# Performance work log

Measured on AMD Instinct MI355X. Metric: run time of the kernel, lower is better.

The kernel has to match this reference:

```python
import jax, jax.numpy as jnp
import numpy as np

V, E, H, L = 50000, 300, 256, 5
B, T_C, T_T = 64, 637, 24


def _lstm_dir(x, wih, whh, b, reverse):
    # x: [B,T,E]; wih: [4H,E]; whh: [4H,H]; b: [4H]
    pre = jnp.einsum('bte,ge->btg', x, wih) + b  # [B,T,4H]
    h0 = jnp.zeros((x.shape[0], whh.shape[1]), x.dtype)

    def step(carry, p):
        h, c = carry
        g = p + h @ whh.T
        i, f, gg, o = jnp.split(g, 4, axis=-1)
        c = jax.nn.sigmoid(f) * c + jax.nn.sigmoid(i) * jnp.tanh(gg)
        h = jax.nn.sigmoid(o) * jnp.tanh(c)
        return (h, c), h

    _, hs = jax.lax.scan(step, (h0, h0), jnp.swapaxes(pre, 0, 1), reverse=reverse)
    return jnp.swapaxes(hs, 0, 1)  # [B,T,H]


def _bilstm(x, wih_f, whh_f, b_f, wih_b, whh_b, b_b):
    return jnp.concatenate([
        _lstm_dir(x, wih_f, whh_f, b_f, False),
        _lstm_dir(x, wih_b, whh_b, b_b, True),
    ], axis=-1)  # [B,T,2H]


def setup_inputs() -> dict:
    key = jax.random.key(0)
    ks = jax.random.split(key, 20)
    k = 1.0 / np.sqrt(H)
    u = lambda kk, shape: jax.random.uniform(kk, shape, jnp.float32, -k, k)
    inp = {
        'content': jax.random.randint(ks[0], (B, T_C), 0, V),
        'title': jax.random.randint(ks[1], (B, T_T), 0, V),
        'embed_w': jax.random.normal(ks[2], (V, E), jnp.float32),
        't_wih_f': u(ks[3], (4 * H, E)), 't_whh_f': u(ks[4], (4 * H, H)), 't_b_f': u(ks[5], (4 * H,)),
        't_wih_b': u(ks[6], (4 * H, E)), 't_whh_b': u(ks[7], (4 * H, H)), 't_b_b': u(ks[8], (4 * H,)),
        'c_wih_f': u(ks[9], (4 * H, E)), 'c_whh_f': u(ks[10], (4 * H, H)), 'c_b_f': u(ks[11], (4 * H,)),
        'c_wih_b': u(ks[12], (4 * H, E)), 'c_whh_b': u(ks[13], (4 * H, H)), 'c_b_b': u(ks[14], (4 * H,)),
        'att_w': u(ks[15], (2 * H, 2 * H)),
        'fc_w': u(ks[16], (L, T_C)), 'fc_b': u(ks[17], (L,)),
    }
    return inp


def reference(content, title, embed_w, t_wih_f, t_whh_f, t_b_f, t_wih_b, t_whh_b, t_b_b,
              c_wih_f, c_whh_f, c_b_f, c_wih_b, c_whh_b, c_b_b, att_w, fc_w, fc_b):
    content_embed = embed_w[content]  # [B,Tc,E]
    title_embed = embed_w[title]      # [B,Tt,E]
    title_rep = _bilstm(title_embed, t_wih_f, t_whh_f, t_b_f, t_wih_b, t_whh_b, t_b_b)
    content_rep = _bilstm(content_embed, c_wih_f, c_whh_f, c_b_f, c_wih_b, c_whh_b, c_b_b)
    title_last = title_rep[:, -1, :]  # [B,2H]
    # score[b,t] = title_last[b] . (att_w @ content_rep[b,t])  (Linear with weight att_w: x @ att_w.T)
    a = jnp.einsum('bj,jk,btk->bt', title_last, att_w, content_rep)  # [B,Tc]
    a = jax.nn.softmax(a, axis=1)
    return jax.nn.log_softmax(a @ fc_w.T + fc_b, axis=1)  # [B,L]
```

## Files before the change

kernel.cpp:

```cpp
#include <hip/hip_runtime.h>
#include <stdint.h>

typedef __attribute__((ext_vector_type(8))) short bf16x8v;
typedef __attribute__((ext_vector_type(4))) float f32x4v;
typedef long long i64;

#define DEV static __device__ __forceinline__

#define B_   64
#define TC_  637
#define TCP_ 638
#define TT_  24
#define E_   300
#define KP_  320
#define H_   256
#define NG_  2048

DEV uint16_t f2bf(float f) {
    uint32_t u = __float_as_uint(f);
    u += 0x7fffu + ((u >> 16) & 1u);
    return (uint16_t)(u >> 16);
}
DEV float bf2f(uint16_t h) { return __uint_as_float(((uint32_t)h) << 16); }
DEV float sigm(float x)  { return __builtin_amdgcn_rcpf(1.f + __builtin_amdgcn_exp2f(x * -1.4426950408889634f)); }
DEV float tanhx(float x) { return 1.f - 2.f*__builtin_amdgcn_rcpf(1.f + __builtin_amdgcn_exp2f(x * 2.8853900817779268f)); }

DEV void gload_lds16(const void* g, void* l) {
    __builtin_amdgcn_global_load_lds((const __attribute__((address_space(1))) uint32_t*)g,
                                     (__attribute__((address_space(3))) uint32_t*)l, 16, 0, 0);
}

__global__ void k_prep(const float* t_wih_f, const float* t_wih_b,
                       const float* t_whh_f,
                       const float* c_wih_f, const float* c_wih_b,
                       const float* c_whh_f, const float* c_whh_b,
                       const float* t_b_f, const float* t_b_b,
                       const float* c_b_f, const float* c_b_b,
                       uint16_t* BwC, uint16_t* BwT, float* biasC, float* biasT,
                       uint32_t* w8CF, uint32_t* w8CB, uint32_t* w8TF)
{
    int tid = blockIdx.x*blockDim.x + threadIdx.x;
    int nth = gridDim.x*blockDim.x;
    for (int i = tid; i < NG_*KP_; i += nth) {
        int n = i / KP_, k = i - n*KP_;
        float vc = 0.f, vt = 0.f;
        if (k < E_) {
            vc = (n < 1024) ? c_wih_f[n*E_+k] : c_wih_b[(n-1024)*E_+k];
            vt = (n < 1024) ? t_wih_f[n*E_+k] : t_wih_b[(n-1024)*E_+k];
        }
        BwC[i] = f2bf(vc); BwT[i] = f2bf(vt);
    }
    for (int i = tid; i < 1024*H_/4; i += nth) {
        int base = i*4;
        uint32_t a, b, c;
        a = (uint32_t)__builtin_amdgcn_cvt_pk_fp8_f32(c_whh_f[base], c_whh_f[base+1], 0, false);
        a = (uint32_t)__builtin_amdgcn_cvt_pk_fp8_f32(c_whh_f[base+2], c_whh_f[base+3], (int)a, true);
        b = (uint32_t)__builtin_amdgcn_cvt_pk_fp8_f32(c_whh_b[base], c_whh_b[base+1], 0, false);
        b = (uint32_t)__builtin_amdgcn_cvt_pk_fp8_f32(c_whh_b[base+2], c_whh_b[base+3], (int)b, true);
        c = (uint32_t)__builtin_amdgcn_cvt_pk_fp8_f32(t_whh_f[base], t_whh_f[base+1], 0, false);
        c = (uint32_t)__builtin_amdgcn_cvt_pk_fp8_f32(t_whh_f[base+2], t_whh_f[base+3], (int)c, true);
        w8CF[i] = a; w8CB[i] = b; w8TF[i] = c;
    }
    for (int i = tid; i < NG_; i += nth) {
        biasC[i] = (i < 1024) ? c_b_f[i] : c_b_b[i-1024];
        biasT[i] = (i < 1024) ? t_b_f[i] : t_b_b[i-1024];
    }
}

__global__ void k_gather(const int* __restrict__ content, const int* __restrict__ title,
                         const float* __restrict__ emb,
                         uint16_t* __restrict__ Ac, uint16_t* __restrict__ At)
{
    int tid = blockIdx.x*blockDim.x + threadIdx.x;
    int nth = gridDim.x*blockDim.x;
    const int CCH = 40832*40;
    const int TCH = 1536*40;
    for (int i = tid; i < CCH + TCH; i += nth) {
        uint16_t* dst; int row, c8; int tok;
        if (i < CCH) {
            row = i / 40; c8 = i - row*40;
            int t = row >> 6, b = row & 63;
            tok = (t < TC_) ? content[b*TC_ + t] : -1;
            dst = Ac + (size_t)row*KP_ + c8*8;
        } else {
            int jx = i - CCH;
            row = jx / 40; c8 = jx - row*40;
            int t = row >> 6, b = row & 63;
            tok = title[b*TT_ + t];
            dst = At + (size_t)row*KP_ + c8*8;
        }
        uint32_t dd[4];
        #pragma unroll
        for (int p = 0; p < 4; ++p) {
            int k = c8*8 + p*2;
            float f0 = (tok >= 0 && k   < E_) ? emb[(size_t)tok*E_ + k]   : 0.f;
            float f1 = (tok >= 0 && k+1 < E_) ? emb[(size_t)tok*E_ + k+1] : 0.f;
            dd[p] = (uint32_t)f2bf(f0) | ((uint32_t)f2bf(f1) << 16);
        }
        uint4 q; q.x = dd[0]; q.y = dd[1]; q.z = dd[2]; q.w = dd[3];
        *(uint4*)dst = q;
    }
}

__global__ __launch_bounds__(256) void k_gemm(const uint16_t* __restrict__ A,
        const uint16_t* __restrict__ Bw, const float* __restrict__ bias,
        uint16_t* __restrict__ prep)
{
    __shared__ __align__(16) uint16_t lA[2][128*32];
    __shared__ __align__(16) uint16_t lB[2][128*32];
    const int tid = threadIdx.x;
    const int l = tid & 63, wv = tid >> 6;
    const int m0 = blockIdx.y * 128, n0 = blockIdx.x * 128;

    auto stage = [&](int kc, int bi) {
        #pragma unroll
        for (int r = 0; r < 2; ++r) {
            int row = r*64 + (tid >> 2);
            int cu  = (tid & 3) * 8;
            gload_lds16(A  + (size_t)(m0 + row)*KP_ + kc*32 + cu, &lA[bi][r*2048 + wv*512]);
            gload_lds16(Bw + (size_t)(n0 + row)*KP_ + kc*32 + cu, &lB[bi][r*2048 + wv*512]);
        }
    };

    f32x4v acc[4][4];
    #pragma unroll
    for (int i = 0; i < 4; ++i)
        #pragma unroll
        for (int j = 0; j < 4; ++j)
            acc[i][j] = f32x4v{0.f,0.f,0.f,0.f};

    const int mtb = (wv >> 1) * 4, ntb = (wv & 1) * 4;

    stage(0, 0);
    __syncthreads();
    for (int kc = 0; kc < 10; ++kc) {
        if (kc < 9) stage(kc + 1, (kc + 1) & 1);
        {
            int bi = kc & 1;
            bf16x8v af[4], bfr[4];
            #pragma unroll
            for (int i = 0; i < 4; ++i) {
                af[i]  = *(const bf16x8v*)&lA[bi][((mtb+i)*16 + (l&15))*32 + (l>>4)*8];
                bfr[i] = *(const bf16x8v*)&lB[bi][((ntb+i)*16 + (l&15))*32 + (l>>4)*8];
            }
            #pragma unroll
            for (int i = 0; i < 4; ++i)
                #pragma unroll
                for (int j = 0; j < 4; ++j)
                    acc[i][j] = __builtin_amdgcn_mfma_f32_16x16x32_bf16(bfr[j], af[i], acc[i][j], 0,0,0);
        }
        __syncthreads();
    }

    const int hi = l >> 4;
    #pragma unroll
    for (int j = 0; j < 4; ++j) {
        int n16 = (n0 >> 4) + ntb + j;
        int dir = n16 >> 6;
        int q   = n16 & 63;
        int ty  = q >> 4;
        int wp  = q & 15;
        float4 bv = *(const float4*)(bias + n16*16 + hi*4);
        #pragma unroll
        for (int i = 0; i < 4; ++i) {
            int rowblk = (m0 >> 4) + mtb + i;
            int t    = rowblk >> 2;
            int bblk = rowblk & 3;
            int unit = t*8 + bblk*2 + dir;
            ushort4 pk;
            pk.x = f2bf(acc[i][j][0] + bv.x);
            pk.y = f2bf(acc[i][j][1] + bv.y);
            pk.z = f2bf(acc[i][j][2] + bv.z);
            pk.w = f2bf(acc[i][j][3] + bv.w);
            size_t off = (size_t)unit*16384 + (size_t)wp*1024 + (size_t)l*16 + ty*4;
            *(ushort4*)(prep + off) = pk;
        }
    }
}

__global__ __launch_bounds__(1024, 4) void k_rnn(
    const uint16_t* __restrict__ preC, const uint16_t* __restrict__ preT,
    const uint8_t* __restrict__ w8CF, const uint8_t* __restrict__ w8CB,
    const uint8_t* __restrict__ w8TF,
    uint16_t* __restrict__ cr, float* __restrict__ tl)
{
    __shared__ __align__(16) char smem[8192];

    const int tid = threadIdx.x;
    const int l = tid & 63, wp = tid >> 6;
    const int m = l & 15, hi = l >> 4;
    const int u = blockIdx.x;

    int dir, bblk, t0, tstep, nsteps, tlOff = -1;
    bool doCR = false;
    const uint16_t* pre; const uint8_t* whh8 = nullptr;
    if (u < 8) {
        dir = u & 1; bblk = u >> 1;
        nsteps = TC_; t0 = dir ? (TC_-1) : 0; tstep = dir ? -1 : 1;
        whh8 = dir ? w8CB : w8CF; pre = preC; doCR = true;
    } else if (u < 12) {
        dir = 0; bblk = u - 8; nsteps = TT_; t0 = 0; tstep = 1;
        whh8 = w8TF; pre = preT; tlOff = 0;
    } else {
        dir = 1; bblk = u - 12; nsteps = 1; t0 = TT_-1; tstep = -1;
        whh8 = nullptr; pre = preT; tlOff = 256;
    }
    const int b0 = bblk * 16;

    i64 w8r[4][8];
    if (whh8) {
        #pragma unroll
        for (int ty = 0; ty < 4; ++ty) {
            int n = ty*256 + wp*16 + m;
            #pragma unroll
            for (int kc = 0; kc < 8; ++kc)
                w8r[ty][kc] = *(const i64*)(whh8 + (size_t)n*H_ + kc*32 + hi*8);
        }
        #pragma unroll
        for (int ty = 0; ty < 4; ++ty)
            #pragma unroll
            for (int kc = 0; kc < 8; ++kc)
                asm volatile("" : "+a"(w8r[ty][kc]));
    }
    for (int i = tid; i < 2048; i += 1024) ((uint32_t*)smem)[i] = 0;
    __syncthreads();

    const int sw = (m & 3) << 5;
    const int rdBase = m*256 + hi*8;
    const int wa = m*256 + (((wp << 4) + hi*4) ^ sw);
    uint16_t* crp = cr + ((size_t)(b0 + m)*TC_ + t0)*512 + dir*256 + (wp << 4) + hi*4;
    const intptr_t crAdv = (intptr_t)tstep * 512;

    float cst[4] = {0.f, 0.f, 0.f, 0.f};

    const uint16_t* pp = pre + (size_t)(t0*8 + bblk*2 + dir)*16384
                             + (size_t)(wp << 10) + (size_t)l*16;
    const intptr_t ppAdv = (intptr_t)tstep * 131072;

    uint4 pf0 = *(const uint4*)(pp);
    uint4 pf1 = *(const uint4*)(pp + 8);

    for (int s = 0; s < nsteps; ++s) {
        const char* hb = (const char*)smem + (s & 1)*4096;
        char*       ho = smem + ((s & 1) ^ 1)*4096;

        f32x4v acc[4];
        acc[0][0]=__uint_as_float(pf0.x<<16); acc[0][1]=__uint_as_float(pf0.x&0xffff0000u);
        acc[0][2]=__uint_as_float(pf0.y<<16); acc[0][3]=__uint_as_float(pf0.y&0xffff0000u);
        acc[1][0]=__uint_as_float(pf0.z<<16); acc[1][1]=__uint_as_float(pf0.z&0xffff0000u);
        acc[1][2]=__uint_as_float(pf0.w<<16); acc[1][3]=__uint_as_float(pf0.w&0xffff0000u);
        acc[2][0]=__uint_as_float(pf1.x<<16); acc[2][1]=__uint_as_float(pf1.x&0xffff0000u);
        acc[2][2]=__uint_as_float(pf1.y<<16); acc[2][3]=__uint_as_float(pf1.y&0xffff0000u);
        acc[3][0]=__uint_as_float(pf1.z<<16); acc[3][1]=__uint_as_float(pf1.z&0xffff0000u);
        acc[3][2]=__uint_as_float(pf1.w<<16); acc[3][3]=__uint_as_float(pf1.w&0xffff0000u);

        if (s + 1 < nsteps) {
            pp += ppAdv;
            pf0 = *(const uint4*)(pp);
            pf1 = *(const uint4*)(pp + 8);
        }

        if (whh8) {
            #pragma unroll
            for (int kc = 0; kc < 8; ++kc) {
                i64 a8 = *(const i64*)(hb + rdBase + ((kc << 5) ^ sw));
                asm("v_mfma_f32_16x16x32_fp8_fp8 %0, %1, %2, %0"
                    : "+v"(acc[0]) : "a"(w8r[0][kc]), "v"(a8));
                asm("v_mfma_f32_16x16x32_fp8_fp8 %0, %1, %2, %0"
                    : "+v"(acc[1]) : "a"(w8r[1][kc]), "v"(a8));
                asm("v_mfma_f32_16x16x32_fp8_fp8 %0, %1, %2, %0"
                    : "+v"(acc[2]) : "a"(w8r[2][kc]), "v"(a8));
                asm("v_mfma_f32_16x16x32_fp8_fp8 %0, %1, %2, %0"
                    : "+v"(acc[3]) : "a"(w8r[3][kc]), "v"(a8));
            }
        }

        float hv0, hv1, hv2, hv3;
        {
            float si, sf, tg, so, cv;
            si = sigm(acc[0][0]); sf = sigm(acc[1][0]); tg = tanhx(acc[2][0]); so = sigm(acc[3][0]);
            cv = sf*cst[0] + si*tg; cst[0] = cv; hv0 = so*tanhx(cv);
            si = sigm(acc[0][1]); sf = sigm(acc[1][1]); tg = tanhx(acc[2][1]); so = sigm(acc[3][1]);
            cv = sf*cst[1] + si*tg; cst[1] = cv; hv1 = so*tanhx(cv);
            si = sigm(acc[0][2]); sf = sigm(acc[1][2]); tg = tanhx(acc[2][2]); so = sigm(acc[3][2]);
            cv = sf*cst[2] + si*tg; cst[2] = cv; hv2 = so*tanhx(cv);
            si = sigm(acc[0][3]); sf = sigm(acc[1][3]); tg = tanhx(acc[2][3]); so = sigm(acc[3][3]);
            cv = sf*cst[3] + si*tg; cst[3] = cv; hv3 = so*tanhx(cv);
        }
        uint32_t p8 = (uint32_t)__builtin_amdgcn_cvt_pk_fp8_f32(hv0, hv1, 0, false);
        p8 = (uint32_t)__builtin_amdgcn_cvt_pk_fp8_f32(hv2, hv3, (int)p8, true);
        *(uint32_t*)(ho + wa) = p8;

        if (doCR) {
            uint32_t b01, b23;
            asm("v_cvt_pk_bf16_f32 %0, %1, %2" : "=v"(b01) : "v"(hv0), "v"(hv1));
            asm("v_cvt_pk_bf16_f32 %0, %1, %2" : "=v"(b23) : "v"(hv2), "v"(hv3));
            uint2 st; st.x = b01; st.y = b23;
            *(uint2*)crp = st;
            crp += crAdv;
        }
        if (tlOff >= 0 && s == nsteps - 1) {
            float4 fv; fv.x = hv0; fv.y = hv1; fv.z = hv2; fv.w = hv3;
            *(float4*)(tl + (size_t)(b0 + m)*512 + tlOff + (wp << 4) + hi*4) = fv;
        }

        __builtin_amdgcn_sched_barrier(0);
        asm volatile("s_waitcnt lgkmcnt(0)" ::: "memory");
        __builtin_amdgcn_s_barrier();
        __builtin_amdgcn_sched_barrier(0);
    }
}

__global__ __launch_bounds__(256) void k_attn(const uint16_t* __restrict__ cr,
        const float* __restrict__ tl, const float* __restrict__ attw,
        const float* __restrict__ fcw, const float* __restrict__ fcb,
        float* __restrict__ out)
{
    __shared__ float sT[512];
    __shared__ float sQ[512];
    __shared__ float sS[640];
    __shared__ float sR[256];
    const int b = blockIdx.x, tid = threadIdx.x;
    for (int i = tid; i < 512; i += 256) sT[i] = tl[(size_t)b*512 + i];
    __syncthreads();
    for (int n = tid; n < 512; n += 256) {
        float s = 0.f;
        for (int j = 0; j < 512; ++j) s += sT[j] * attw[(size_t)j*512 + n];
        sQ[n] = s;
    }
    __syncthreads();
    for (int t = tid; t < TC_; t += 256) {
        const uint16_t* row = cr + ((size_t)b*TC_ + t)*512;
        float s = 0.f;
        for (int c = 0; c < 64; ++c) {
            uint4 v = *(const uint4*)(row + c*8);
            uint32_t d;
            d = v.x; s += bf2f((uint16_t)(d&0xffff))*sQ[c*8+0] + bf2f((uint16_t)(d>>16))*sQ[c*8+1];
            d = v.y; s += bf2f((uint16_t)(d&0xffff))*sQ[c*8+2] + bf2f((uint16_t)(d>>16))*sQ[c*8+3];
            d = v.z; s += bf2f((uint16_t)(d&0xffff))*sQ[c*8+4] + bf2f((uint16_t)(d>>16))*sQ[c*8+5];
            d = v.w; s += bf2f((uint16_t)(d&0xffff))*sQ[c*8+6] + bf2f((uint16_t)(d>>16))*sQ[c*8+7];
        }
        sS[t] = s;
    }
    __syncthreads();
    float lm = -1e30f;
    for (int t = tid; t < TC_; t += 256) lm = fmaxf(lm, sS[t]);
    sR[tid] = lm; __syncthreads();
    for (int o = 128; o > 0; o >>= 1) { if (tid < o) sR[tid] = fmaxf(sR[tid], sR[tid+o]); __syncthreads(); }
    float M = sR[0]; __syncthreads();
    float ls = 0.f;
    for (int t = tid; t < TC_; t += 256) { float e = __expf(sS[t]-M); sS[t] = e; ls += e; }
    sR[tid] = ls; __syncthreads();
    for (int o = 128; o > 0; o >>= 1) { if (tid < o) sR[tid] += sR[tid+o]; __syncthreads(); }
    float inv = 1.f / sR[0]; __syncthreads();
    float la[5] = {0.f,0.f,0.f,0.f,0.f};
    for (int t = tid; t < TC_; t += 256) {
        float p = sS[t] * inv;
        #pragma unroll
        for (int ll = 0; ll < 5; ++ll) la[ll] += p * fcw[ll*TC_ + t];
    }
    float lg[5];
    #pragma unroll
    for (int ll = 0; ll < 5; ++ll) {
        sR[tid] = la[ll]; __syncthreads();
        for (int o = 128; o > 0; o >>= 1) { if (tid < o) sR[tid] += sR[tid+o]; __syncthreads(); }
        lg[ll] = sR[0] + fcb[ll]; __syncthreads();
    }
    if (tid == 0) {
        float m2 = lg[0];
        #pragma unroll
        for (int ll = 1; ll < 5; ++ll) m2 = fmaxf(m2, lg[ll]);
        float se = 0.f;
        #pragma unroll
        for (int ll = 0; ll < 5; ++ll) se += __expf(lg[ll] - m2);
        float lse = __logf(se) + m2;
        #pragma unroll
        for (int ll = 0; ll < 5; ++ll) out[b*5 + ll] = lg[ll] - lse;
    }
}

extern "C" void kernel_launch(void* const* d_in, const int* in_sizes, int n_in,
                              void* d_out, int out_size, void* d_ws, size_t ws_size,
                              hipStream_t stream)
{
    const int*   content = (const int*)d_in[0];
    const int*   title   = (const int*)d_in[1];
    const float* embed_w = (const float*)d_in[2];
    const float* t_wih_f = (const float*)d_in[3];
    const float* t_whh_f = (const float*)d_in[4];
    const float* t_b_f   = (const float*)d_in[5];
    const float* t_wih_b = (const float*)d_in[6];
    const float* t_b_b   = (const float*)d_in[8];
    const float* c_wih_f = (const float*)d_in[9];
    const float* c_whh_f = (const float*)d_in[10];
    const float* c_b_f   = (const float*)d_in[11];
    const float* c_wih_b = (const float*)d_in[12];
    const float* c_whh_b = (const float*)d_in[13];
    const float* c_b_b   = (const float*)d_in[14];
    const float* att_w   = (const float*)d_in[15];
    const float* fc_w    = (const float*)d_in[16];
    const float* fc_b    = (const float*)d_in[17];
    float* out = (float*)d_out;

    char* ws = (char*)d_ws;
    size_t o = 0;
    auto alloc = [&](size_t sz) { char* p = ws + o; o = (o + sz + 255) & ~(size_t)255; return p; };
    uint16_t* Ac    = (uint16_t*)alloc((size_t)40832*KP_*2);
    uint16_t* At    = (uint16_t*)alloc((size_t)1536*KP_*2);
    uint16_t* BwC   = (uint16_t*)alloc((size_t)NG_*KP_*2);
    uint16_t* BwT   = (uint16_t*)alloc((size_t)NG_*KP_*2);
    float*    biasC = (float*)   alloc((size_t)NG_*4);
    float*    biasT = (float*)   alloc((size_t)NG_*4);
    uint8_t*  w8CF  = (uint8_t*) alloc((size_t)1024*H_);
    uint8_t*  w8CB  = (uint8_t*) alloc((size_t)1024*H_);
    uint8_t*  w8TF  = (uint8_t*) alloc((size_t)1024*H_);
    uint16_t* preC  = (uint16_t*)alloc((size_t)TCP_*262144);
    uint16_t* preT  = (uint16_t*)alloc((size_t)TT_*262144);
    uint16_t* crp   = (uint16_t*)alloc((size_t)B_*TC_*512*2);
    float*    tlp   = (float*)   alloc((size_t)B_*512*4);

    k_prep<<<256, 256, 0, stream>>>(t_wih_f, t_wih_b, t_whh_f, c_wih_f, c_wih_b,
                                    c_whh_f, c_whh_b, t_b_f, t_b_b, c_b_f, c_b_b,
                                    BwC, BwT, biasC, biasT,
                                    (uint32_t*)w8CF, (uint32_t*)w8CB, (uint32_t*)w8TF);
    k_gather<<<2048, 256, 0, stream>>>(content, title, embed_w, Ac, At);
    k_gemm<<<dim3(16, 319), 256, 0, stream>>>(Ac, BwC, biasC, preC);
    k_gemm<<<dim3(16, 12),  256, 0, stream>>>(At, BwT, biasT, preT);
    k_rnn<<<16, 1024, 0, stream>>>(preC, preT, w8CF, w8CB, w8TF, crp, tlp);
    k_attn<<<64, 256, 0, stream>>>(crp, tlp, att_w, fc_w, fc_b, out);
}
```

Baseline: 1.696 ms.

## Widen LDS hidden-state reads and fuse LSTM gate math into fewer transcendentals

Changes the fp8 hidden-state LDS layout so each lane fetches two k-chunks with one 16-byte read, using a new swizzle matched by a new write address. This halves the LDS read instructions in the MFMA loop. The gate math is rewritten algebraically: the sigmoids and tanh are combined into shared reciprocals, with two exp2-based rcp calls per element instead of many separate rcp calls. This shortens the serial per-step latency of the recurrence, at the cost of a clamp on the cell value inside tanh and possible overflow or precision changes in the products of exponentials.

```diff
diff --git a/kernel.cpp b/kernel.cpp
--- a/kernel.cpp
+++ b/kernel.cpp
@@ -4,6 +4,7 @@
 typedef __attribute__((ext_vector_type(8))) short bf16x8v;
 typedef __attribute__((ext_vector_type(4))) float f32x4v;
 typedef long long i64;
+typedef __attribute__((ext_vector_type(2))) long long i64x2;
 
 #define DEV static __device__ __forceinline__
 
@@ -225,9 +226,13 @@
     for (int i = tid; i < 2048; i += 1024) ((uint32_t*)smem)[i] = 0;
     __syncthreads();
 
-    const int sw = (m & 3) << 5;
-    const int rdBase = m*256 + hi*8;
-    const int wa = m*256 + (((wp << 4) + hi*4) ^ sw);
+    int rda[4];
+    #pragma unroll
+    for (int q = 0; q < 4; ++q) rda[q] = m*256 + hi*64 + (((q ^ (m & 3))) << 4);
+    const int waddr = m*256 + (((wp*2 + (hi >> 1)) & 3) << 6)
+                    + ((((wp >> 2) ^ (m & 3))) << 4)
+                    + (((wp >> 1) & 1) << 3) + ((hi & 1) << 2);
+
     uint16_t* crp = cr + ((size_t)(b0 + m)*TC_ + t0)*512 + dir*256 + (wp << 4) + hi*4;
     const intptr_t crAdv = (intptr_t)tstep * 512;
 
@@ -239,6 +244,9 @@
 
     uint4 pf0 = *(const uint4*)(pp);
     uint4 pf1 = *(const uint4*)(pp + 8);
+
+    const float KN = -1.4426950408889634f;
+    const float K2 =  2.8853900817779268f;
 
     for (int s = 0; s < nsteps; ++s) {
         const char* hb = (const char*)smem + (s & 1)*4096;
@@ -262,45 +270,60 @@
 
         if (whh8) {
             #pragma unroll
-            for (int kc = 0; kc < 8; ++kc) {
-                i64 a8 = *(const i64*)(hb + rdBase + ((kc << 5) ^ sw));
-                asm("v_mfma_f32_16x16x32_fp8_fp8 %0, %1, %2, %0"
-                    : "+v"(acc[0]) : "a"(w8r[0][kc]), "v"(a8));
-                asm("v_mfma_f32_16x16x32_fp8_fp8 %0, %1, %2, %0"
-                    : "+v"(acc[1]) : "a"(w8r[1][kc]), "v"(a8));
-                asm("v_mfma_f32_16x16x32_fp8_fp8 %0, %1, %2, %0"
-                    : "+v"(acc[2]) : "a"(w8r[2][kc]), "v"(a8));
-                asm("v_mfma_f32_16x16x32_fp8_fp8 %0, %1, %2, %0"
-                    : "+v"(acc[3]) : "a"(w8r[3][kc]), "v"(a8));
+            for (int q = 0; q < 4; ++q) {
+                i64x2 a = *(const i64x2*)(hb + rda[q]);
+                asm("v_mfma_f32_16x16x32_fp8_fp8 %0, %1, %2, %0"
+                    : "+v"(acc[0]) : "a"(w8r[0][2*q]), "v"(a[0]));
+                asm("v_mfma_f32_16x16x32_fp8_fp8 %0, %1, %2, %0"
+                    : "+v"(acc[1]) : "a"(w8r[1][2*q]), "v"(a[0]));
+                asm("v_mfma_f32_16x16x32_fp8_fp8 %0, %1, %2, %0"
+                    : "+v"(acc[2]) : "a"(w8r[2][2*q]), "v"(a[0]));
+                asm("v_mfma_f32_16x16x32_fp8_fp8 %0, %1, %2, %0"
+                    : "+v"(acc[3]) : "a"(w8r[3][2*q]), "v"(a[0]));
+                asm("v_mfma_f32_16x16x32_fp8_fp8 %0, %1, %2, %0"
+                    : "+v"(acc[0]) : "a"(w8r[0][2*q+1]), "v"(a[1]));
+                asm("v_mfma_f32_16x16x32_fp8_fp8 %0, %1, %2, %0"
+                    : "+v"(acc[1]) : "a"(w8r[1][2*q+1]), "v"(a[1]));
+                asm("v_mfma_f32_16x16x32_fp8_fp8 %0, %1, %2, %0"
+                    : "+v"(acc[2]) : "a"(w8r[2][2*q+1]), "v"(a[1]));
+                asm("v_mfma_f32_16x16x32_fp8_fp8 %0, %1, %2, %0"
+                    : "+v"(acc[3]) : "a"(w8r[3][2*q+1]), "v"(a[1]));
             }
         }
 
-        float hv0, hv1, hv2, hv3;
-        {
-            float si, sf, tg, so, cv;
-            si = sigm(acc[0][0]); sf = sigm(acc[1][0]); tg = tanhx(acc[2][0]); so = sigm(acc[3][0]);
-            cv = sf*cst[0] + si*tg; cst[0] = cv; hv0 = so*tanhx(cv);
-            si = sigm(acc[0][1]); sf = sigm(acc[1][1]); tg = tanhx(acc[2][1]); so = sigm(acc[3][1]);
-            cv = sf*cst[1] + si*tg; cst[1] = cv; hv1 = so*tanhx(cv);
-            si = sigm(acc[0][2]); sf = sigm(acc[1][2]); tg = tanhx(acc[2][2]); so = sigm(acc[3][2]);
-            cv = sf*cst[2] + si*tg; cst[2] = cv; hv2 = so*tanhx(cv);
-            si = sigm(acc[0][3]); sf = sigm(acc[1][3]); tg = tanhx(acc[2][3]); so = sigm(acc[3][3]);
-            cv = sf*cst[3] + si*tg; cst[3] = cv; hv3 = so*tanhx(cv);
-        }
-        uint32_t p8 = (uint32_t)__builtin_amdgcn_cvt_pk_fp8_f32(hv0, hv1, 0, false);
-        p8 = (uint32_t)__builtin_amdgcn_cvt_pk_fp8_f32(hv2, hv3, (int)p8, true);
-        *(uint32_t*)(ho + wa) = p8;
+        float hv[4];
+        #pragma unroll
+        for (int r = 0; r < 4; ++r) {
+            float Ei = __builtin_amdgcn_exp2f(acc[0][r] * KN);
+            float Ef = __builtin_amdgcn_exp2f(acc[1][r] * KN);
+            float Eg = __builtin_amdgcn_exp2f(acc[2][r] * (2.f*KN));
+            float Eo = __builtin_amdgcn_exp2f(acc[3][r] * KN);
+            float A  = 1.f + Ei;
+            float Bb = 1.f + Eg;
+            float C  = 1.f + Ef;
+            float AB = A * Bb;
+            float num = __builtin_fmaf(cst[r], AB, (2.f - Bb) * C);
+            float cv  = num * __builtin_amdgcn_rcpf(AB * C);
+            cst[r] = cv;
+            float cc = fminf(fmaxf(cv, -15.f), 15.f);
+            float P  = __builtin_amdgcn_exp2f(cc * K2);
+            hv[r] = (P - 1.f) * __builtin_amdgcn_rcpf((1.f + Eo) * (P + 1.f));
+        }
+
+        uint32_t p8 = (uint32_t)__builtin_amdgcn_cvt_pk_fp8_f32(hv[0], hv[1], 0, false);
+        p8 = (uint32_t)__builtin_amdgcn_cvt_pk_fp8_f32(hv[2], hv[3], (int)p8, true);
+        *(uint32_t*)(ho + waddr) = p8;
 
         if (doCR) {
             uint32_t b01, b23;
-            asm("v_cvt_pk_bf16_f32 %0, %1, %2" : "=v"(b01) : "v"(hv0), "v"(hv1));
-            asm("v_cvt_pk_bf16_f32 %0, %1, %2" : "=v"(b23) : "v"(hv2), "v"(hv3));
+            asm("v_cvt_pk_bf16_f32 %0, %1, %2" : "=v"(b01) : "v"(hv[0]), "v"(hv[1]));
+            asm("v_cvt_pk_bf16_f32 %0, %1, %2" : "=v"(b23) : "v"(hv[2]), "v"(hv[3]));
             uint2 st; st.x = b01; st.y = b23;
             *(uint2*)crp = st;
             crp += crAdv;
         }
         if (tlOff >= 0 && s == nsteps - 1) {
-            float4 fv; fv.x = hv0; fv.y = hv1; fv.z = hv2; fv.w = hv3;
+            float4 fv; fv.x = hv[0]; fv.y = hv[1]; fv.z = hv[2]; fv.w = hv[3];
             *(float4*)(tl + (size_t)(b0 + m)*512 + tlOff + (wp << 4) + hi*4) = fv;
         }
 
```

Result: faster. 1.463 ms (-13.7%).
